# Optimization experiments

Measured on AMD Instinct MI355X. Metric: run time of the kernel, lower is better.

The kernel has to match this reference:

```python
import jax, jax.numpy as jnp
import numpy as np

B, T, C = 2, 2048, 2048
H, HKV = 32, 8
D = C // H            # head_dim = 64
G = H // HKV          # groups = 4
ROPE_BASE = 10000.0


def _rotate_half(x):
    x1, x2 = jnp.split(x, 2, axis=-1)
    return jnp.concatenate((-x2, x1), axis=-1)


def _rope_tables(seq_len, dim):
    inv_freq = 1.0 / (ROPE_BASE ** (jnp.arange(0, dim, 2, dtype=jnp.float32) / dim))
    t = jnp.arange(seq_len, dtype=jnp.float32)
    freqs = jnp.outer(t, inv_freq)          # [T, D/2]
    emb = jnp.concatenate((freqs, freqs), axis=-1)  # [T, D]
    return jnp.cos(emb), jnp.sin(emb)


def setup_inputs() -> dict:
    key = jax.random.key(0)
    ks = jax.random.split(key, 5)
    s = 0.02
    return {
        "x": jax.random.normal(ks[0], (B, T, C), jnp.float32),
        "Wq": jax.random.normal(ks[1], (C, C), jnp.float32) * s,
        "Wk": jax.random.normal(ks[2], (HKV * D, C), jnp.float32) * s,
        "Wv": jax.random.normal(ks[3], (HKV * D, C), jnp.float32) * s,
        "Wo": jax.random.normal(ks[4], (C, C), jnp.float32) * s,
    }


def reference(x, Wq, Wk, Wv, Wo):
    b, t, c = x.shape
    # fused QKV projections (nn.Linear: y = x @ W.T)
    q = (x @ Wq.T).reshape(b, t, H, D).transpose(0, 2, 1, 3)      # [B,H,T,D]
    k = (x @ Wk.T).reshape(b, t, HKV, D).transpose(0, 2, 1, 3)    # [B,HKV,T,D]
    v = (x @ Wv.T).reshape(b, t, HKV, D).transpose(0, 2, 1, 3)

    # RoPE (start_pos = 0)
    cos, sin = _rope_tables(t, D)           # [T, D] each
    cos = cos[None, None]                   # [1,1,T,D]
    sin = sin[None, None]
    q = q * cos + _rotate_half(q) * sin
    k = k * cos + _rotate_half(k) * sin

    # GQA head expansion (repeat_interleave on head dim)
    k = jnp.repeat(k, G, axis=1)            # [B,H,T,D]
    v = jnp.repeat(v, G, axis=1)

    # causal attention
    scale = 1.0 / jnp.sqrt(jnp.asarray(D, jnp.float32))
    scores = jnp.einsum('bhqd,bhkd->bhqk', q, k) * scale          # [B,H,T,T]
    causal = jnp.tril(jnp.ones((t, t), dtype=bool))
    scores = jnp.where(causal[None, None], scores, -jnp.inf)
    attn = jax.nn.softmax(scores.astype(jnp.float32), axis=-1).astype(q.dtype)
    out = jnp.einsum('bhqk,bhkd->bhqd', attn, v)                  # [B,H,T,D]
    out = out.transpose(0, 2, 1, 3).reshape(b, t, c)
    return out @ Wo.T
```

## Files before the change

### kernel.cpp

```cpp
#include <hip/hip_runtime.h>
#include <hip/hip_bf16.h>
#include <math.h>

typedef short short8 __attribute__((ext_vector_type(8)));
typedef float floatx4 __attribute__((ext_vector_type(4)));
typedef unsigned int uintx4 __attribute__((ext_vector_type(4)));
typedef int intx2 __attribute__((ext_vector_type(2)));

typedef __attribute__((address_space(1))) unsigned int as1_u32;
typedef __attribute__((address_space(3))) unsigned int as3_u32;

__device__ __forceinline__ void load_lds16(const void* g, void* l) {
  __builtin_amdgcn_global_load_lds((const as1_u32*)g, (as3_u32*)l, 16, 0, 0);
}

__device__ __forceinline__ unsigned short f2bf(float f) {
  __bf16 h = (__bf16)f;
  return __builtin_bit_cast(unsigned short, h);
}

__device__ __forceinline__ unsigned int pack_bf16(float a, float b) {
  return (unsigned int)f2bf(a) | ((unsigned int)f2bf(b) << 16);
}

#define TB 2
#define TT 2048
#define TC 2048
#define QKN 2560
#define KOFF 2048
#define SCALE_Q 0.18033688f

__global__ __launch_bounds__(256) void cast_all(
    const float* __restrict__ x, const float* __restrict__ wq,
    const float* __restrict__ wk, const float* __restrict__ wv,
    const float* __restrict__ wo,
    unsigned short* __restrict__ xb, unsigned short* __restrict__ wqkv,
    unsigned short* __restrict__ wob, float2* __restrict__ ropeTab) {
  if (blockIdx.x < 256) {
    const int idx = blockIdx.x * 256 + threadIdx.x;
    const int t = idx >> 5, d = idx & 31;
    const float inv = exp2f((float)d * -0.4152410119f);
    float sn, cs;
    sincosf((float)t * inv, &sn, &cs);
    ropeTab[idx] = make_float2(cs, sn);
  }
  long i4 = (long)blockIdx.x * 256 + threadIdx.x;
  const float* src;
  unsigned short* dst;
  if (i4 < 2097152)      { src = x;  dst = xb; }
  else if (i4 < 3145728) { src = wq; dst = wqkv;           i4 -= 2097152; }
  else if (i4 < 3407872) { src = wk; dst = wqkv + 4194304; i4 -= 3145728; }
  else if (i4 < 3670016) { src = wv; dst = wqkv + 5242880; i4 -= 3407872; }
  else                   { src = wo; dst = wob;            i4 -= 3670016; }
  float4 v = ((const float4*)src)[i4];
  ushort4 o;
  o.x = f2bf(v.x); o.y = f2bf(v.y); o.z = f2bf(v.z); o.w = f2bf(v.w);
  ((ushort4*)dst)[i4] = o;
}

__global__ __launch_bounds__(256) void gemm_qkv(const unsigned short* __restrict__ A,
                                                const unsigned short* __restrict__ Bw,
                                                unsigned short* __restrict__ qk,
                                                unsigned short* __restrict__ vT,
                                                const float2* __restrict__ ropeTab) {
  __shared__ unsigned short As[128 * 64];
  __shared__ unsigned short Bs[128 * 64];
  const int K = 2048;
  const int tid = threadIdx.x;
  const int lane = tid & 63, w = tid >> 6;
  const int quad = lane >> 4, l15 = lane & 15;
  const int wm = w >> 1, wn = w & 1;
  const int lin = blockIdx.y * 24 + blockIdx.x;
  const int sub = lin >> 3;
  const int m0 = (sub / 3) * 128;
  const int n0 = ((lin & 7) * 3 + sub % 3) * 128;

  floatx4 acc[4][4];
#pragma unroll
  for (int i = 0; i < 4; ++i)
#pragma unroll
    for (int j = 0; j < 4; ++j) acc[i][j] = (floatx4){0.f, 0.f, 0.f, 0.f};

  const int ar = tid >> 3;
  const int ac = (((tid & 7) ^ (ar & 7)) * 8);
  const unsigned short* Abase = A + (size_t)(m0 + ar) * K + ac;
  const unsigned short* Bbase = Bw + (size_t)(n0 + ar) * K + ac;

  for (int k0 = 0; k0 < K; k0 += 64) {
    __syncthreads();
#pragma unroll
    for (int p = 0; p < 4; ++p) {
      load_lds16(Abase + (size_t)(p * 32) * K + k0, (char*)As + p * 4096 + tid * 16);
      load_lds16(Bbase + (size_t)(p * 32) * K + k0, (char*)Bs + p * 4096 + tid * 16);
    }
    __syncthreads();
#pragma unroll
    for (int ks = 0; ks < 2; ++ks) {
      short8 af[4], bfr[4];
      const int key = (((ks << 2) + quad) ^ (l15 & 7)) << 4;
#pragma unroll
      for (int i = 0; i < 4; ++i)
        af[i] = *(const short8*)((const char*)As + (wm * 64 + i * 16 + l15) * 128 + key);
#pragma unroll
      for (int j = 0; j < 4; ++j)
        bfr[j] = *(const short8*)((const char*)Bs + (wn * 64 + j * 16 + l15) * 128 + key);
#pragma unroll
      for (int i = 0; i < 4; ++i)
#pragma unroll
        for (int j = 0; j < 4; ++j)
          acc[i][j] = __builtin_amdgcn_mfma_f32_16x16x32_bf16(af[i], bfr[j], acc[i][j], 0, 0, 0);
    }
  }

  const int colb = n0 + wn * 64;
  if (colb < QKN) {
    const float qscale = (colb < KOFF) ? SCALE_Q : 1.0f;
#pragma unroll
    for (int i = 0; i < 4; ++i) {
      const int rowb = m0 + wm * 64 + i * 16 + quad * 4;
      const int tb = rowb & (TT - 1);
#pragma unroll
      for (int j = 0; j < 2; ++j) {
        const int col = colb + j * 16 + l15;
        const int d = j * 16 + l15;
#pragma unroll
        for (int r = 0; r < 4; ++r) {
          const float2 cssn = ropeTab[(tb + r) * 32 + d];
          const float a = acc[i][j][r], b2 = acc[i][j + 2][r];
          const float qa = (a * cssn.x - b2 * cssn.y) * qscale;
          const float qb = (b2 * cssn.x + a * cssn.y) * qscale;
          unsigned short* p = qk + (size_t)(rowb + r) * QKN + col;
          p[0] = f2bf(qa);
          p[32] = f2bf(qb);
        }
      }
    }
  } else {
#pragma unroll
    for (int i = 0; i < 4; ++i) {
      const int rowb = m0 + wm * 64 + i * 16 + quad * 4;
#pragma unroll
      for (int j = 0; j < 4; ++j) {
        const int col = colb + j * 16 + l15;
        ushort4 pk;
        pk.x = f2bf(acc[i][j][0]); pk.y = f2bf(acc[i][j][1]);
        pk.z = f2bf(acc[i][j][2]); pk.w = f2bf(acc[i][j][3]);
        *(ushort4*)(vT + (size_t)(col - 2560) * 4096 + rowb) = pk;
      }
    }
  }
}

__global__ __launch_bounds__(256) void gemm_nt_f32(const unsigned short* __restrict__ A,
                                                   const unsigned short* __restrict__ Bw,
                                                   float* __restrict__ C,
                                                   int M, int N, int K) {
  __shared__ unsigned short As[128 * 64];
  __shared__ unsigned short Bs[128 * 64];
  const int tid = threadIdx.x;
  const int lane = tid & 63, w = tid >> 6;
  const int quad = lane >> 4, l15 = lane & 15;
  const int wm = w >> 1, wn = w & 1;
  const int lin = blockIdx.y * 16 + blockIdx.x;
  const int sub = lin >> 3;
  const int m0 = (sub >> 1) * 128;
  const int n0 = ((lin & 7) * 2 + (sub & 1)) * 128;

  floatx4 acc[4][4];
#pragma unroll
  for (int i = 0; i < 4; ++i)
#pragma unroll
    for (int j = 0; j < 4; ++j) acc[i][j] = (floatx4){0.f, 0.f, 0.f, 0.f};

  const int ar = tid >> 3;
  const int ac = (((tid & 7) ^ (ar & 7)) * 8);
  const unsigned short* Abase = A + (size_t)(m0 + ar) * K + ac;
  const unsigned short* Bbase = Bw + (size_t)(n0 + ar) * K + ac;

  for (int k0 = 0; k0 < K; k0 += 64) {
    __syncthreads();
#pragma unroll
    for (int p = 0; p < 4; ++p) {
      load_lds16(Abase + (size_t)(p * 32) * K + k0, (char*)As + p * 4096 + tid * 16);
      load_lds16(Bbase + (size_t)(p * 32) * K + k0, (char*)Bs + p * 4096 + tid * 16);
    }
    __syncthreads();
#pragma unroll
    for (int ks = 0; ks < 2; ++ks) {
      short8 af[4], bfr[4];
      const int key = (((ks << 2) + quad) ^ (l15 & 7)) << 4;
#pragma unroll
      for (int i = 0; i < 4; ++i)
        af[i] = *(const short8*)((const char*)As + (wm * 64 + i * 16 + l15) * 128 + key);
#pragma unroll
      for (int j = 0; j < 4; ++j)
        bfr[j] = *(const short8*)((const char*)Bs + (wn * 64 + j * 16 + l15) * 128 + key);
#pragma unroll
      for (int i = 0; i < 4; ++i)
#pragma unroll
        for (int j = 0; j < 4; ++j)
          acc[i][j] = __builtin_amdgcn_mfma_f32_16x16x32_bf16(af[i], bfr[j], acc[i][j], 0, 0, 0);
    }
  }
#pragma unroll
  for (int i = 0; i < 4; ++i) {
    const int row = m0 + wm * 64 + i * 16 + quad * 4;
#pragma unroll
    for (int j = 0; j < 4; ++j) {
      const int col = n0 + wn * 64 + j * 16 + l15;
#pragma unroll
      for (int r = 0; r < 4; ++r)
        C[(size_t)(row + r) * N + col] = acc[i][j][r];
    }
  }
}

__global__ __launch_bounds__(256, 3) void attn_kernel(const unsigned short* __restrict__ qk,
                                                      const unsigned short* __restrict__ vT,
                                                      unsigned short* __restrict__ attn) {
  const int h = blockIdx.x, b = blockIdx.y;
  const int qt = 15 - (int)blockIdx.z;
  const int hk = h >> 2;
  const int tid = threadIdx.x;
  const int w = tid >> 6, lane = tid & 63, quad = lane >> 4, l15 = lane & 15;

  __shared__ char lds[32768];

  const int srow = tid >> 3;
  const int sgrp = ((tid & 7) ^ (srow & 7));
  const int relbase = w * 32 + l15;

  const short8 ones = {16256, 16256, 16256, 16256, 16256, 16256, 16256, 16256};

  const size_t rowQ = (size_t)(b * TT + qt * 128);

  {
    const unsigned short* qsrc = qk + (rowQ + srow) * QKN + h * 64 + sgrp * 8;
#pragma unroll
    for (int p = 0; p < 4; ++p)
      load_lds16(qsrc + (size_t)p * 32 * QKN, lds + p * 4096 + tid * 16);
  }
  __syncthreads();
  short8 qf[2][2];
#pragma unroll
  for (int i = 0; i < 2; ++i)
#pragma unroll
    for (int ks = 0; ks < 2; ++ks)
      qf[i][ks] = *(const short8*)(lds + (w * 32 + i * 16 + l15) * 128 +
                                   ((((ks << 2) + quad) ^ (l15 & 7)) << 4));
  __syncthreads();

  floatx4 accO[2][4], accL[2];
#pragma unroll
  for (int i = 0; i < 2; ++i) {
    accL[i] = (floatx4){0.f, 0.f, 0.f, 0.f};
#pragma unroll
    for (int j = 0; j < 4; ++j) accO[i][j] = (floatx4){0.f, 0.f, 0.f, 0.f};
  }

  const unsigned short* kptr =
      qk + (size_t)(b * TT + srow) * QKN + KOFF + hk * 64 + sgrp * 8;
  const unsigned short* vptr =
      vT + (size_t)(hk * 64 + srow) * 4096 + b * TT + sgrp * 8;

  load_lds16(kptr, lds + tid * 16);
  load_lds16(kptr + (size_t)32 * QKN, lds + 4096 + tid * 16);
  load_lds16(vptr, lds + 16384 + tid * 16);
  load_lds16(vptr + (size_t)32 * 4096, lds + 16384 + 4096 + tid * 16);
  kptr += (size_t)64 * QKN;
  vptr += 64;
  __syncthreads();

  auto step = [&](const int BUF, const bool PREF, const int MREL) {
    if (PREF) {
      char* kd = lds + ((BUF ^ 1) * 8192);
      char* vd = lds + 16384 + ((BUF ^ 1) * 8192);
      load_lds16(kptr, kd + tid * 16);
      load_lds16(kptr + (size_t)32 * QKN, kd + 4096 + tid * 16);
      load_lds16(vptr, vd + tid * 16);
      load_lds16(vptr + (size_t)32 * 4096, vd + 4096 + tid * 16);
      kptr += (size_t)64 * QKN;
      vptr += 64;
    }

    const char* Ks = lds + BUF * 8192;
    floatx4 st[2][4];
    __builtin_amdgcn_s_setprio(1);
#pragma unroll
    for (int jm = 0; jm < 4; ++jm) {
      const int krow = jm * 16 + l15;
      const short8 kf0 = *(const short8*)(Ks + krow * 128 + ((quad ^ (l15 & 7)) << 4));
      const short8 kf1 = *(const short8*)(Ks + krow * 128 + (((4 + quad) ^ (l15 & 7)) << 4));
#pragma unroll
      for (int i = 0; i < 2; ++i) {
        floatx4 z = (floatx4){0.f, 0.f, 0.f, 0.f};
        z = __builtin_amdgcn_mfma_f32_16x16x32_bf16(kf0, qf[i][0], z, 0, 0, 0);
        st[i][jm] = __builtin_amdgcn_mfma_f32_16x16x32_bf16(kf1, qf[i][1], z, 0, 0, 0);
      }
    }
    __builtin_amdgcn_s_setprio(0);

    const char* Vt = lds + 16384 + BUF * 8192;
    short8 vf[2][4];
#pragma unroll
    for (int ks = 0; ks < 2; ++ks)
#pragma unroll
      for (int jd = 0; jd < 4; ++jd) {
        const int d = jd * 16 + l15;
        vf[ks][jd] = *(const short8*)(Vt + d * 128 +
                                      ((((ks << 2) + quad) ^ (l15 & 7)) << 4));
      }

    short8 pT[2][2];
#pragma unroll
    for (int i = 0; i < 2; ++i) {
      unsigned int U[4][2];
#pragma unroll
      for (int jm = 0; jm < 4; ++jm) {
        float e0 = exp2f(st[i][jm][0]);
        float e1 = exp2f(st[i][jm][1]);
        float e2 = exp2f(st[i][jm][2]);
        float e3 = exp2f(st[i][jm][3]);
        if (MREL >= 0) {
          const int rel = relbase + i * 16 - MREL;
          const int kg = jm * 16 + quad * 4;
          if (kg > rel) e0 = 0.f;
          if (kg + 1 > rel) e1 = 0.f;
          if (kg + 2 > rel) e2 = 0.f;
          if (kg + 3 > rel) e3 = 0.f;
        }
        U[jm][0] = pack_bf16(e0, e1);
        U[jm][1] = pack_bf16(e2, e3);
      }
#pragma unroll
      for (int ks = 0; ks < 2; ++ks) {
        uintx4 t;
#pragma unroll
        for (int hh = 0; hh < 2; ++hh) {
          intx2 r32 = __builtin_amdgcn_permlane32_swap(
              (int)U[2 * ks][hh], (int)U[2 * ks + 1][hh], false, false);
          intx2 r16 = __builtin_amdgcn_permlane16_swap(r32[0], r32[1], false, false);
          t[hh] = (unsigned int)r16[0];
          t[2 + hh] = (unsigned int)r16[1];
        }
        pT[i][ks] = __builtin_bit_cast(short8, t);
      }
    }

    __builtin_amdgcn_s_setprio(1);
#pragma unroll
    for (int ks = 0; ks < 2; ++ks) {
      accL[0] = __builtin_amdgcn_mfma_f32_16x16x32_bf16(pT[0][ks], ones, accL[0], 0, 0, 0);
      accL[1] = __builtin_amdgcn_mfma_f32_16x16x32_bf16(pT[1][ks], ones, accL[1], 0, 0, 0);
#pragma unroll
      for (int jd = 0; jd < 4; ++jd) {
        accO[0][jd] = __builtin_amdgcn_mfma_f32_16x16x32_bf16(pT[0][ks], vf[ks][jd], accO[0][jd], 0, 0, 0);
        accO[1][jd] = __builtin_amdgcn_mfma_f32_16x16x32_bf16(pT[1][ks], vf[ks][jd], accO[1][jd], 0, 0, 0);
      }
    }
    __builtin_amdgcn_s_setprio(0);
    __syncthreads();
  };

  for (int t2 = 0; t2 < qt; ++t2) {
    step(0, true, -1);
    step(1, true, -1);
  }
  step(0, true, 0);
  step(1, false, 64);

#pragma unroll
  for (int i2 = 0; i2 < 2; ++i2) {
#pragma unroll
    for (int jd = 0; jd < 4; ++jd) {
      const int col = h * 64 + jd * 16 + l15;
#pragma unroll
      for (int r = 0; r < 4; ++r) {
        const size_t row = rowQ + w * 32 + i2 * 16 + quad * 4 + r;
        attn[row * TC + col] = f2bf(accO[i2][jd][r] / accL[i2][r]);
      }
    }
  }
}

extern "C" void kernel_launch(void* const* d_in, const int* in_sizes, int n_in,
                              void* d_out, int out_size, void* d_ws, size_t ws_size,
                              hipStream_t stream) {
  const float* x = (const float*)d_in[0];
  const float* Wq = (const float*)d_in[1];
  const float* Wk = (const float*)d_in[2];
  const float* Wv = (const float*)d_in[3];
  const float* Wo = (const float*)d_in[4];
  float* out = (float*)d_out;

  char* ws = (char*)d_ws;
  unsigned short* xb   = (unsigned short*)(ws);
  unsigned short* wqkv = (unsigned short*)(ws + 16777216);
  unsigned short* wob  = (unsigned short*)(ws + 29360128);
  unsigned short* qk   = (unsigned short*)(ws + 37748736);
  unsigned short* vT   = (unsigned short*)(ws + 58720256);
  unsigned short* attn = (unsigned short*)(ws + 62914560);
  float2* ropeTab = (float2*)(ws + 62914560);

  cast_all<<<18432, 256, 0, stream>>>(x, Wq, Wk, Wv, Wo, xb, wqkv, wob, ropeTab);
  gemm_qkv<<<dim3(24, 32), 256, 0, stream>>>(xb, wqkv, qk, vT, ropeTab);
  attn_kernel<<<dim3(32, 2, 16), 256, 0, stream>>>(qk, vT, attn);
  gemm_nt_f32<<<dim3(16, 32), 256, 0, stream>>>(attn, wob, out, 4096, TC, 2048);
}
```

Baseline: 295.8 us.

## Rewrite projection GEMMs with 256x256 tiles and a 4-stage async LDS pipeline

Both the QKV and output-projection GEMMs move from 128x128 tiles with 256 threads and a single-buffered, two-barrier K loop to 256x256 tiles with 512 threads. They now use a four-buffer ring in 128KB of dynamic LDS, K-steps of 32, and `global_load_lds` prefetched three stages ahead. Explicit vmcnt waits and one barrier per stage replace the old sync pattern, and s_setprio raises wave priority around the MFMA blocks. The goal is to overlap global loads with MFMA work and cut LDS traffic per FLOP. The cost is far fewer workgroups (192 and 128) on a 256-CU part, so fewer CUs are kept busy.

```diff
diff --git a/kernel.cpp b/kernel.cpp
--- a/kernel.cpp
+++ b/kernel.cpp
@@ -58,66 +58,94 @@
   ((ushort4*)dst)[i4] = o;
 }
 
-__global__ __launch_bounds__(256) void gemm_qkv(const unsigned short* __restrict__ A,
-                                                const unsigned short* __restrict__ Bw,
-                                                unsigned short* __restrict__ qk,
-                                                unsigned short* __restrict__ vT,
-                                                const float2* __restrict__ ropeTab) {
-  __shared__ unsigned short As[128 * 64];
-  __shared__ unsigned short Bs[128 * 64];
-  const int K = 2048;
+
+__global__ __launch_bounds__(512, 2) void gemm_qkv(const unsigned short* __restrict__ A,
+                                                   const unsigned short* __restrict__ Bw,
+                                                   unsigned short* __restrict__ qk,
+                                                   unsigned short* __restrict__ vT,
+                                                   const float2* __restrict__ ropeTab) {
+  extern __shared__ char dynlds[];
+  const int K = 2048, NTILES = 64;
   const int tid = threadIdx.x;
   const int lane = tid & 63, w = tid >> 6;
   const int quad = lane >> 4, l15 = lane & 15;
-  const int wm = w >> 1, wn = w & 1;
-  const int lin = blockIdx.y * 24 + blockIdx.x;
-  const int sub = lin >> 3;
-  const int m0 = (sub / 3) * 128;
-  const int n0 = ((lin & 7) * 3 + sub % 3) * 128;
-
-  floatx4 acc[4][4];
-#pragma unroll
-  for (int i = 0; i < 4; ++i)
+  const int wm = w >> 2, wn = w & 3;
+
+  const int lin = blockIdx.y * 12 + blockIdx.x;
+  const int wg = (lin & 7) * 24 + (lin >> 3);
+  const int m0 = (wg / 12) * 256;
+  const int n0 = (wg % 12) * 256;
+
+  floatx4 acc[8][4];
+#pragma unroll
+  for (int i = 0; i < 8; ++i)
 #pragma unroll
     for (int j = 0; j < 4; ++j) acc[i][j] = (floatx4){0.f, 0.f, 0.f, 0.f};
 
-  const int ar = tid >> 3;
-  const int ac = (((tid & 7) ^ (ar & 7)) * 8);
-  const unsigned short* Abase = A + (size_t)(m0 + ar) * K + ac;
-  const unsigned short* Bbase = Bw + (size_t)(n0 + ar) * K + ac;
-
-  for (int k0 = 0; k0 < K; k0 += 64) {
-    __syncthreads();
-#pragma unroll
-    for (int p = 0; p < 4; ++p) {
-      load_lds16(Abase + (size_t)(p * 32) * K + k0, (char*)As + p * 4096 + tid * 16);
-      load_lds16(Bbase + (size_t)(p * 32) * K + k0, (char*)Bs + p * 4096 + tid * 16);
-    }
-    __syncthreads();
-#pragma unroll
-    for (int ks = 0; ks < 2; ++ks) {
-      short8 af[4], bfr[4];
-      const int key = (((ks << 2) + quad) ^ (l15 & 7)) << 4;
-#pragma unroll
-      for (int i = 0; i < 4; ++i)
-        af[i] = *(const short8*)((const char*)As + (wm * 64 + i * 16 + l15) * 128 + key);
+  const int srow = tid >> 2;
+  const int schk = (tid & 3) ^ (srow & 3);
+  const unsigned short* aS = A + (size_t)(m0 + srow) * K + schk * 8;
+  const unsigned short* bS = Bw + (size_t)(n0 + srow) * K + schk * 8;
+
+  const int rsw = (quad ^ (l15 & 3)) << 4;
+  const int rdA = (wm * 128 + l15) * 64 + rsw;
+  const int rdB = (wn * 64 + l15) * 64 + rsw;
+
+#pragma unroll
+  for (int tt = 0; tt < 3; ++tt) {
+    char* sb = dynlds + tt * 32768;
+    const unsigned short* aP = aS + (size_t)tt * 32;
+    const unsigned short* bP = bS + (size_t)tt * 32;
+    load_lds16(aP, sb + tid * 16);
+    load_lds16(aP + (size_t)128 * K, sb + 8192 + tid * 16);
+    load_lds16(bP, sb + 16384 + tid * 16);
+    load_lds16(bP + (size_t)128 * K, sb + 24576 + tid * 16);
+  }
+
+  auto kiter = [&](int t, const int VN, const bool ISSUE) {
+    if (VN == 8)      asm volatile("s_waitcnt vmcnt(8)" ::: "memory");
+    else if (VN == 4) asm volatile("s_waitcnt vmcnt(4)" ::: "memory");
+    else              asm volatile("s_waitcnt vmcnt(0)" ::: "memory");
+    __builtin_amdgcn_s_barrier();
+    asm volatile("" ::: "memory");
+    if (ISSUE) {
+      const int tt = t + 3;
+      char* sb = dynlds + (tt & 3) * 32768;
+      const unsigned short* aP = aS + (size_t)tt * 32;
+      const unsigned short* bP = bS + (size_t)tt * 32;
+      load_lds16(aP, sb + tid * 16);
+      load_lds16(aP + (size_t)128 * K, sb + 8192 + tid * 16);
+      load_lds16(bP, sb + 16384 + tid * 16);
+      load_lds16(bP + (size_t)128 * K, sb + 24576 + tid * 16);
+    }
+    const char* cb = dynlds + (t & 3) * 32768;
+    short8 af[8], bf[4];
+#pragma unroll
+    for (int i = 0; i < 8; ++i)
+      af[i] = *(const short8*)(cb + rdA + i * 1024);
+#pragma unroll
+    for (int j = 0; j < 4; ++j)
+      bf[j] = *(const short8*)(cb + 16384 + rdB + j * 1024);
+    __builtin_amdgcn_s_setprio(1);
+#pragma unroll
+    for (int i = 0; i < 8; ++i)
 #pragma unroll
       for (int j = 0; j < 4; ++j)
-        bfr[j] = *(const short8*)((const char*)Bs + (wn * 64 + j * 16 + l15) * 128 + key);
-#pragma unroll
-      for (int i = 0; i < 4; ++i)
-#pragma unroll
-        for (int j = 0; j < 4; ++j)
-          acc[i][j] = __builtin_amdgcn_mfma_f32_16x16x32_bf16(af[i], bfr[j], acc[i][j], 0, 0, 0);
-    }
-  }
+        acc[i][j] = __builtin_amdgcn_mfma_f32_16x16x32_bf16(af[i], bf[j], acc[i][j], 0, 0, 0);
+    __builtin_amdgcn_s_setprio(0);
+  };
+
+  for (int t = 0; t < NTILES - 3; ++t) kiter(t, 8, true);
+  kiter(NTILES - 3, 8, false);
+  kiter(NTILES - 2, 4, false);
+  kiter(NTILES - 1, 0, false);
 
   const int colb = n0 + wn * 64;
   if (colb < QKN) {
     const float qscale = (colb < KOFF) ? SCALE_Q : 1.0f;
 #pragma unroll
-    for (int i = 0; i < 4; ++i) {
-      const int rowb = m0 + wm * 64 + i * 16 + quad * 4;
+    for (int i = 0; i < 8; ++i) {
+      const int rowb = m0 + wm * 128 + i * 16 + quad * 4;
       const int tb = rowb & (TT - 1);
 #pragma unroll
       for (int j = 0; j < 2; ++j) {
@@ -137,8 +165,8 @@
     }
   } else {
 #pragma unroll
-    for (int i = 0; i < 4; ++i) {
-      const int rowb = m0 + wm * 64 + i * 16 + quad * 4;
+    for (int i = 0; i < 8; ++i) {
+      const int rowb = m0 + wm * 128 + i * 16 + quad * 4;
 #pragma unroll
       for (int j = 0; j < 4; ++j) {
         const int col = colb + j * 16 + l15;
@@ -151,60 +179,89 @@
   }
 }
 
-__global__ __launch_bounds__(256) void gemm_nt_f32(const unsigned short* __restrict__ A,
-                                                   const unsigned short* __restrict__ Bw,
-                                                   float* __restrict__ C,
-                                                   int M, int N, int K) {
-  __shared__ unsigned short As[128 * 64];
-  __shared__ unsigned short Bs[128 * 64];
+__global__ __launch_bounds__(512, 2) void gemm_nt_f32(const unsigned short* __restrict__ A,
+                                                      const unsigned short* __restrict__ Bw,
+                                                      float* __restrict__ C,
+                                                      int M, int N, int Kdim) {
+  extern __shared__ char dynlds[];
+  const int K = 2048, NTILES = 64;
   const int tid = threadIdx.x;
   const int lane = tid & 63, w = tid >> 6;
   const int quad = lane >> 4, l15 = lane & 15;
-  const int wm = w >> 1, wn = w & 1;
-  const int lin = blockIdx.y * 16 + blockIdx.x;
-  const int sub = lin >> 3;
-  const int m0 = (sub >> 1) * 128;
-  const int n0 = ((lin & 7) * 2 + (sub & 1)) * 128;
-
-  floatx4 acc[4][4];
-#pragma unroll
-  for (int i = 0; i < 4; ++i)
+  const int wm = w >> 2, wn = w & 3;
+
+  const int lin = blockIdx.y * 8 + blockIdx.x;
+  const int wg = (lin & 7) * 16 + (lin >> 3);
+  const int m0 = (wg >> 3) * 256;
+  const int n0 = (wg & 7) * 256;
+
+  floatx4 acc[8][4];
+#pragma unroll
+  for (int i = 0; i < 8; ++i)
 #pragma unroll
     for (int j = 0; j < 4; ++j) acc[i][j] = (floatx4){0.f, 0.f, 0.f, 0.f};
 
-  const int ar = tid >> 3;
-  const int ac = (((tid & 7) ^ (ar & 7)) * 8);
-  const unsigned short* Abase = A + (size_t)(m0 + ar) * K + ac;
-  const unsigned short* Bbase = Bw + (size_t)(n0 + ar) * K + ac;
-
-  for (int k0 = 0; k0 < K; k0 += 64) {
-    __syncthreads();
-#pragma unroll
-    for (int p = 0; p < 4; ++p) {
-      load_lds16(Abase + (size_t)(p * 32) * K + k0, (char*)As + p * 4096 + tid * 16);
-      load_lds16(Bbase + (size_t)(p * 32) * K + k0, (char*)Bs + p * 4096 + tid * 16);
-    }
-    __syncthreads();
-#pragma unroll
-    for (int ks = 0; ks < 2; ++ks) {
-      short8 af[4], bfr[4];
-      const int key = (((ks << 2) + quad) ^ (l15 & 7)) << 4;
-#pragma unroll
-      for (int i = 0; i < 4; ++i)
-        af[i] = *(const short8*)((const char*)As + (wm * 64 + i * 16 + l15) * 128 + key);
+  const int srow = tid >> 2;
+  const int schk = (tid & 3) ^ (srow & 3);
+  const unsigned short* aS = A + (size_t)(m0 + srow) * K + schk * 8;
+  const unsigned short* bS = Bw + (size_t)(n0 + srow) * K + schk * 8;
+
+  const int rsw = (quad ^ (l15 & 3)) << 4;
+  const int rdA = (wm * 128 + l15) * 64 + rsw;
+  const int rdB = (wn * 64 + l15) * 64 + rsw;
+
+#pragma unroll
+  for (int tt = 0; tt < 3; ++tt) {
+    char* sb = dynlds + tt * 32768;
+    const unsigned short* aP = aS + (size_t)tt * 32;
+    const unsigned short* bP = bS + (size_t)tt * 32;
+    load_lds16(aP, sb + tid * 16);
+    load_lds16(aP + (size_t)128 * K, sb + 8192 + tid * 16);
+    load_lds16(bP, sb + 16384 + tid * 16);
+    load_lds16(bP + (size_t)128 * K, sb + 24576 + tid * 16);
+  }
+
+  auto kiter = [&](int t, const int VN, const bool ISSUE) {
+    if (VN == 8)      asm volatile("s_waitcnt vmcnt(8)" ::: "memory");
+    else if (VN == 4) asm volatile("s_waitcnt vmcnt(4)" ::: "memory");
+    else              asm volatile("s_waitcnt vmcnt(0)" ::: "memory");
+    __builtin_amdgcn_s_barrier();
+    asm volatile("" ::: "memory");
+    if (ISSUE) {
+      const int tt = t + 3;
+      char* sb = dynlds + (tt & 3) * 32768;
+      const unsigned short* aP = aS + (size_t)tt * 32;
+      const unsigned short* bP = bS + (size_t)tt * 32;
+      load_lds16(aP, sb + tid * 16);
+      load_lds16(aP + (size_t)128 * K, sb + 8192 + tid * 16);
+      load_lds16(bP, sb + 16384 + tid * 16);
+      load_lds16(bP + (size_t)128 * K, sb + 24576 + tid * 16);
+    }
+    const char* cb = dynlds + (t & 3) * 32768;
+    short8 af[8], bf[4];
+#pragma unroll
+    for (int i = 0; i < 8; ++i)
+      af[i] = *(const short8*)(cb + rdA + i * 1024);
+#pragma unroll
+    for (int j = 0; j < 4; ++j)
+      bf[j] = *(const short8*)(cb + 16384 + rdB + j * 1024);
+    __builtin_amdgcn_s_setprio(1);
+#pragma unroll
+    for (int i = 0; i < 8; ++i)
 #pragma unroll
       for (int j = 0; j < 4; ++j)
-        bfr[j] = *(const short8*)((const char*)Bs + (wn * 64 + j * 16 + l15) * 128 + key);
-#pragma unroll
-      for (int i = 0; i < 4; ++i)
-#pragma unroll
-        for (int j = 0; j < 4; ++j)
-          acc[i][j] = __builtin_amdgcn_mfma_f32_16x16x32_bf16(af[i], bfr[j], acc[i][j], 0, 0, 0);
-    }
-  }
-#pragma unroll
-  for (int i = 0; i < 4; ++i) {
-    const int row = m0 + wm * 64 + i * 16 + quad * 4;
+        acc[i][j] = __builtin_amdgcn_mfma_f32_16x16x32_bf16(af[i], bf[j], acc[i][j], 0, 0, 0);
+    __builtin_amdgcn_s_setprio(0);
+  };
+
+  for (int t = 0; t < NTILES - 3; ++t) kiter(t, 8, true);
+  kiter(NTILES - 3, 8, false);
+  kiter(NTILES - 2, 4, false);
+  kiter(NTILES - 1, 0, false);
+
+#pragma unroll
+  for (int i = 0; i < 8; ++i) {
+    const int row = m0 + wm * 128 + i * 16 + quad * 4;
 #pragma unroll
     for (int j = 0; j < 4; ++j) {
       const int col = n0 + wn * 64 + j * 16 + l15;
@@ -403,7 +460,7 @@
   float2* ropeTab = (float2*)(ws + 62914560);
 
   cast_all<<<18432, 256, 0, stream>>>(x, Wq, Wk, Wv, Wo, xb, wqkv, wob, ropeTab);
-  gemm_qkv<<<dim3(24, 32), 256, 0, stream>>>(xb, wqkv, qk, vT, ropeTab);
+  gemm_qkv<<<dim3(12, 16), 512, 131072, stream>>>(xb, wqkv, qk, vT, ropeTab);
   attn_kernel<<<dim3(32, 2, 16), 256, 0, stream>>>(qk, vT, attn);
-  gemm_nt_f32<<<dim3(16, 32), 256, 0, stream>>>(attn, wob, out, 4096, TC, 2048);
-}
+  gemm_nt_f32<<<dim3(8, 16), 512, 131072, stream>>>(attn, wob, out, 4096, TC, 2048);
+}
```

New measurement: 299.2 us. About the same (+1.1%).

## Replace GEMMs with 256x256-tile double-buffered 8-wave phased MFMA pipeline

Applied to the files above, without the earlier changes.

Both projection GEMMs now share a helper that computes 256x256 output tiles with 512 threads. It double-buffers 128KB of dynamic LDS and splits each k-step into four phases, so global-to-LDS loads of the next tile overlap MFMA work on the current one, with explicit waitcnt, barriers and setprio. The larger tiles cut global traffic per flop, and the grid is remapped to match. The cost is far fewer workgroups (192 and 128 blocks), which may underfill the CUs, plus heavy register and LDS use and many barriers.

```diff
diff --git a/kernel.cpp b/kernel.cpp
--- a/kernel.cpp
+++ b/kernel.cpp
@@ -22,6 +22,8 @@
 __device__ __forceinline__ unsigned int pack_bf16(float a, float b) {
   return (unsigned int)f2bf(a) | ((unsigned int)f2bf(b) << 16);
 }
+
+#define MFMA16(a, b, c) __builtin_amdgcn_mfma_f32_16x16x32_bf16(a, b, c, 0, 0, 0)
 
 #define TB 2
 #define TT 2048
@@ -58,75 +60,167 @@
   ((ushort4*)dst)[i4] = o;
 }
 
-__global__ __launch_bounds__(256) void gemm_qkv(const unsigned short* __restrict__ A,
-                                                const unsigned short* __restrict__ Bw,
-                                                unsigned short* __restrict__ qk,
-                                                unsigned short* __restrict__ vT,
-                                                const float2* __restrict__ ropeTab) {
-  __shared__ unsigned short As[128 * 64];
-  __shared__ unsigned short Bs[128 * 64];
+__device__ __forceinline__ void gemm256_8ph(
+    const unsigned short* __restrict__ A, const unsigned short* __restrict__ Bw,
+    char* dynlds, int m0, int n0, int K, floatx4 (&acc)[8][4]) {
+  const int tid = threadIdx.x;
+  const int lane = tid & 63;
+  const int w = tid >> 6;
+  const int quad = lane >> 4, l15 = lane & 15;
+  const int wm = w >> 2, wn = w & 3;
+
+  const int srow8 = tid >> 3;
+  const int schk = (tid & 7) ^ (srow8 & 7);
+  const unsigned short* aS = A + (size_t)(m0 + srow8) * K + schk * 8;
+  const unsigned short* bS = Bw + (size_t)(n0 + srow8) * K + schk * 8;
+
+  const int key0 = (quad ^ (l15 & 7)) << 4;
+  const int key1 = ((4 + quad) ^ (l15 & 7)) << 4;
+  const int rdA = (wm * 16 + l15) * 128;
+  const int rdB = 32768 + ((wn >> 1) * 64 + (wn & 1) * 16 + l15) * 128;
+
+  const int NT = K >> 6;
+
+  auto stage = [&](int bb, int isB, int h, int tt) {
+    char* d = dynlds + bb * 65536 + isB * 32768 + h * 16384;
+    const unsigned short* s = (isB ? bS : aS) + (size_t)tt * 64 + (size_t)(h * 128) * K;
+    load_lds16(s, d + tid * 16);
+    load_lds16(s + (size_t)64 * K, d + 8192 + tid * 16);
+  };
+
+  stage(0, 0, 0, 0); stage(0, 1, 0, 0); stage(0, 1, 1, 0); stage(0, 0, 1, 0);
+  asm volatile("s_waitcnt vmcnt(4)" ::: "memory");
+  __builtin_amdgcn_s_barrier();
+
+  for (int t = 0; t < NT; ++t) {
+    const int b = t & 1, nb = b ^ 1;
+    const char* cb = dynlds + b * 65536;
+    const bool STG = (t < NT - 1);
+    short8 af[4][2], bfA[2][2], bfB[2][2];
+
+#pragma unroll
+    for (int i = 0; i < 4; ++i) {
+      af[i][0] = *(const short8*)(cb + rdA + i * 4096 + key0);
+      af[i][1] = *(const short8*)(cb + rdA + i * 4096 + key1);
+    }
+#pragma unroll
+    for (int j = 0; j < 2; ++j) {
+      bfA[j][0] = *(const short8*)(cb + rdB + j * 4096 + key0);
+      bfA[j][1] = *(const short8*)(cb + rdB + j * 4096 + key1);
+    }
+    if (STG) {
+      stage(nb, 0, 0, t + 1); stage(nb, 1, 0, t + 1);
+      asm volatile("s_waitcnt vmcnt(4)" ::: "memory");
+    } else {
+      asm volatile("s_waitcnt vmcnt(0)" ::: "memory");
+    }
+    __builtin_amdgcn_s_barrier();
+    asm volatile("s_waitcnt lgkmcnt(0)" ::: "memory");
+    __builtin_amdgcn_s_setprio(1);
+#pragma unroll
+    for (int i = 0; i < 4; ++i)
+#pragma unroll
+      for (int j = 0; j < 2; ++j) {
+        acc[i][j] = MFMA16(af[i][0], bfA[j][0], acc[i][j]);
+        acc[i][j] = MFMA16(af[i][1], bfA[j][1], acc[i][j]);
+      }
+    __builtin_amdgcn_s_setprio(0);
+    __builtin_amdgcn_s_barrier();
+
+#pragma unroll
+    for (int j = 0; j < 2; ++j) {
+      bfB[j][0] = *(const short8*)(cb + rdB + 16384 + j * 4096 + key0);
+      bfB[j][1] = *(const short8*)(cb + rdB + 16384 + j * 4096 + key1);
+    }
+    __builtin_amdgcn_s_barrier();
+    asm volatile("s_waitcnt lgkmcnt(0)" ::: "memory");
+    __builtin_amdgcn_s_setprio(1);
+#pragma unroll
+    for (int i = 0; i < 4; ++i)
+#pragma unroll
+      for (int j = 0; j < 2; ++j) {
+        acc[i][j + 2] = MFMA16(af[i][0], bfB[j][0], acc[i][j + 2]);
+        acc[i][j + 2] = MFMA16(af[i][1], bfB[j][1], acc[i][j + 2]);
+      }
+    __builtin_amdgcn_s_setprio(0);
+    __builtin_amdgcn_s_barrier();
+
+#pragma unroll
+    for (int i = 0; i < 4; ++i) {
+      af[i][0] = *(const short8*)(cb + rdA + (i + 4) * 4096 + key0);
+      af[i][1] = *(const short8*)(cb + rdA + (i + 4) * 4096 + key1);
+    }
+    if (STG) { stage(nb, 1, 1, t + 1); stage(nb, 0, 1, t + 1); }
+    __builtin_amdgcn_s_barrier();
+    asm volatile("s_waitcnt lgkmcnt(0)" ::: "memory");
+    __builtin_amdgcn_s_setprio(1);
+#pragma unroll
+    for (int i = 0; i < 4; ++i)
+#pragma unroll
+      for (int j = 0; j < 2; ++j) {
+        acc[i + 4][j + 2] = MFMA16(af[i][0], bfB[j][0], acc[i + 4][j + 2]);
+        acc[i + 4][j + 2] = MFMA16(af[i][1], bfB[j][1], acc[i + 4][j + 2]);
+      }
+    __builtin_amdgcn_s_setprio(0);
+    __builtin_amdgcn_s_barrier();
+
+    if (STG) asm volatile("s_waitcnt vmcnt(4)" ::: "memory");
+    __builtin_amdgcn_s_barrier();
+    __builtin_amdgcn_s_setprio(1);
+#pragma unroll
+    for (int i = 0; i < 4; ++i)
+#pragma unroll
+      for (int j = 0; j < 2; ++j) {
+        acc[i + 4][j] = MFMA16(af[i][0], bfA[j][0], acc[i + 4][j]);
+        acc[i + 4][j] = MFMA16(af[i][1], bfA[j][1], acc[i + 4][j]);
+      }
+    __builtin_amdgcn_s_setprio(0);
+    __builtin_amdgcn_s_barrier();
+  }
+}
+
+#define OUTCOL(n0, wn, j, l15) \
+  ((n0) + ((j) >> 1) * 128 + ((wn) >> 1) * 64 + ((wn) & 1) * 16 + ((j) & 1) * 32 + (l15))
+
+__global__ __launch_bounds__(512, 2) void gemm_qkv(const unsigned short* __restrict__ A,
+                                                   const unsigned short* __restrict__ Bw,
+                                                   unsigned short* __restrict__ qk,
+                                                   unsigned short* __restrict__ vT,
+                                                   const float2* __restrict__ ropeTab) {
+  extern __shared__ char dynlds[];
   const int K = 2048;
   const int tid = threadIdx.x;
   const int lane = tid & 63, w = tid >> 6;
   const int quad = lane >> 4, l15 = lane & 15;
-  const int wm = w >> 1, wn = w & 1;
-  const int lin = blockIdx.y * 24 + blockIdx.x;
-  const int sub = lin >> 3;
-  const int m0 = (sub / 3) * 128;
-  const int n0 = ((lin & 7) * 3 + sub % 3) * 128;
-
-  floatx4 acc[4][4];
-#pragma unroll
-  for (int i = 0; i < 4; ++i)
+  const int wm = w >> 2, wn = w & 3;
+
+  const int lin = blockIdx.y * 12 + blockIdx.x;
+  const int wg = (lin & 7) * 24 + (lin >> 3);
+  const int m0 = (wg / 12) * 256;
+  const int n0 = (wg % 12) * 256;
+
+  floatx4 acc[8][4];
+#pragma unroll
+  for (int i = 0; i < 8; ++i)
 #pragma unroll
     for (int j = 0; j < 4; ++j) acc[i][j] = (floatx4){0.f, 0.f, 0.f, 0.f};
 
-  const int ar = tid >> 3;
-  const int ac = (((tid & 7) ^ (ar & 7)) * 8);
-  const unsigned short* Abase = A + (size_t)(m0 + ar) * K + ac;
-  const unsigned short* Bbase = Bw + (size_t)(n0 + ar) * K + ac;
-
-  for (int k0 = 0; k0 < K; k0 += 64) {
-    __syncthreads();
-#pragma unroll
-    for (int p = 0; p < 4; ++p) {
-      load_lds16(Abase + (size_t)(p * 32) * K + k0, (char*)As + p * 4096 + tid * 16);
-      load_lds16(Bbase + (size_t)(p * 32) * K + k0, (char*)Bs + p * 4096 + tid * 16);
-    }
-    __syncthreads();
-#pragma unroll
-    for (int ks = 0; ks < 2; ++ks) {
-      short8 af[4], bfr[4];
-      const int key = (((ks << 2) + quad) ^ (l15 & 7)) << 4;
-#pragma unroll
-      for (int i = 0; i < 4; ++i)
-        af[i] = *(const short8*)((const char*)As + (wm * 64 + i * 16 + l15) * 128 + key);
-#pragma unroll
-      for (int j = 0; j < 4; ++j)
-        bfr[j] = *(const short8*)((const char*)Bs + (wn * 64 + j * 16 + l15) * 128 + key);
-#pragma unroll
-      for (int i = 0; i < 4; ++i)
-#pragma unroll
-        for (int j = 0; j < 4; ++j)
-          acc[i][j] = __builtin_amdgcn_mfma_f32_16x16x32_bf16(af[i], bfr[j], acc[i][j], 0, 0, 0);
-    }
-  }
-
-  const int colb = n0 + wn * 64;
-  if (colb < QKN) {
-    const float qscale = (colb < KOFF) ? SCALE_Q : 1.0f;
-#pragma unroll
-    for (int i = 0; i < 4; ++i) {
-      const int rowb = m0 + wm * 64 + i * 16 + quad * 4;
+  gemm256_8ph(A, Bw, dynlds, m0, n0, K, acc);
+
+  if (n0 < QKN) {
+    const float qscale = (n0 < KOFF) ? SCALE_Q : 1.0f;
+    const int d = (wn & 1) * 16 + l15;
+#pragma unroll
+    for (int i = 0; i < 8; ++i) {
+      const int rowb = m0 + i * 32 + wm * 16 + quad * 4;
       const int tb = rowb & (TT - 1);
 #pragma unroll
-      for (int j = 0; j < 2; ++j) {
-        const int col = colb + j * 16 + l15;
-        const int d = j * 16 + l15;
+      for (int jp = 0; jp < 4; jp += 2) {
+        const int col = OUTCOL(n0, wn, jp, l15);
 #pragma unroll
         for (int r = 0; r < 4; ++r) {
           const float2 cssn = ropeTab[(tb + r) * 32 + d];
-          const float a = acc[i][j][r], b2 = acc[i][j + 2][r];
+          const float a = acc[i][jp][r], b2 = acc[i][jp + 1][r];
           const float qa = (a * cssn.x - b2 * cssn.y) * qscale;
           const float qb = (b2 * cssn.x + a * cssn.y) * qscale;
           unsigned short* p = qk + (size_t)(rowb + r) * QKN + col;
@@ -137,11 +231,11 @@
     }
   } else {
 #pragma unroll
-    for (int i = 0; i < 4; ++i) {
-      const int rowb = m0 + wm * 64 + i * 16 + quad * 4;
+    for (int i = 0; i < 8; ++i) {
+      const int rowb = m0 + i * 32 + wm * 16 + quad * 4;
 #pragma unroll
       for (int j = 0; j < 4; ++j) {
-        const int col = colb + j * 16 + l15;
+        const int col = OUTCOL(n0, wn, j, l15);
         ushort4 pk;
         pk.x = f2bf(acc[i][j][0]); pk.y = f2bf(acc[i][j][1]);
         pk.z = f2bf(acc[i][j][2]); pk.w = f2bf(acc[i][j][3]);
@@ -151,63 +245,36 @@
   }
 }
 
-__global__ __launch_bounds__(256) void gemm_nt_f32(const unsigned short* __restrict__ A,
-                                                   const unsigned short* __restrict__ Bw,
-                                                   float* __restrict__ C,
-                                                   int M, int N, int K) {
-  __shared__ unsigned short As[128 * 64];
-  __shared__ unsigned short Bs[128 * 64];
+__global__ __launch_bounds__(512, 2) void gemm_nt_f32(const unsigned short* __restrict__ A,
+                                                      const unsigned short* __restrict__ Bw,
+                                                      float* __restrict__ C,
+                                                      int M, int N, int Kdim) {
+  extern __shared__ char dynlds[];
+  const int K = 2048;
   const int tid = threadIdx.x;
   const int lane = tid & 63, w = tid >> 6;
   const int quad = lane >> 4, l15 = lane & 15;
-  const int wm = w >> 1, wn = w & 1;
-  const int lin = blockIdx.y * 16 + blockIdx.x;
-  const int sub = lin >> 3;
-  const int m0 = (sub >> 1) * 128;
-  const int n0 = ((lin & 7) * 2 + (sub & 1)) * 128;
-
-  floatx4 acc[4][4];
-#pragma unroll
-  for (int i = 0; i < 4; ++i)
+  const int wm = w >> 2, wn = w & 3;
+
+  const int lin = blockIdx.y * 8 + blockIdx.x;
+  const int wg = (lin & 7) * 16 + (lin >> 3);
+  const int m0 = (wg >> 3) * 256;
+  const int n0 = (wg & 7) * 256;
+
+  floatx4 acc[8][4];
+#pragma unroll
+  for (int i = 0; i < 8; ++i)
 #pragma unroll
     for (int j = 0; j < 4; ++j) acc[i][j] = (floatx4){0.f, 0.f, 0.f, 0.f};
 
-  const int ar = tid >> 3;
-  const int ac = (((tid & 7) ^ (ar & 7)) * 8);
-  const unsigned short* Abase = A + (size_t)(m0 + ar) * K + ac;
-  const unsigned short* Bbase = Bw + (size_t)(n0 + ar) * K + ac;
-
-  for (int k0 = 0; k0 < K; k0 += 64) {
-    __syncthreads();
-#pragma unroll
-    for (int p = 0; p < 4; ++p) {
-      load_lds16(Abase + (size_t)(p * 32) * K + k0, (char*)As + p * 4096 + tid * 16);
-      load_lds16(Bbase + (size_t)(p * 32) * K + k0, (char*)Bs + p * 4096 + tid * 16);
-    }
-    __syncthreads();
-#pragma unroll
-    for (int ks = 0; ks < 2; ++ks) {
-      short8 af[4], bfr[4];
-      const int key = (((ks << 2) + quad) ^ (l15 & 7)) << 4;
-#pragma unroll
-      for (int i = 0; i < 4; ++i)
-        af[i] = *(const short8*)((const char*)As + (wm * 64 + i * 16 + l15) * 128 + key);
-#pragma unroll
-      for (int j = 0; j < 4; ++j)
-        bfr[j] = *(const short8*)((const char*)Bs + (wn * 64 + j * 16 + l15) * 128 + key);
-#pragma unroll
-      for (int i = 0; i < 4; ++i)
-#pragma unroll
-        for (int j = 0; j < 4; ++j)
-          acc[i][j] = __builtin_amdgcn_mfma_f32_16x16x32_bf16(af[i], bfr[j], acc[i][j], 0, 0, 0);
-    }
-  }
-#pragma unroll
-  for (int i = 0; i < 4; ++i) {
-    const int row = m0 + wm * 64 + i * 16 + quad * 4;
+  gemm256_8ph(A, Bw, dynlds, m0, n0, K, acc);
+
+#pragma unroll
+  for (int i = 0; i < 8; ++i) {
+    const int row = m0 + i * 32 + wm * 16 + quad * 4;
 #pragma unroll
     for (int j = 0; j < 4; ++j) {
-      const int col = n0 + wn * 64 + j * 16 + l15;
+      const int col = OUTCOL(n0, wn, j, l15);
 #pragma unroll
       for (int r = 0; r < 4; ++r)
         C[(size_t)(row + r) * N + col] = acc[i][j][r];
@@ -403,7 +470,7 @@
   float2* ropeTab = (float2*)(ws + 62914560);
 
   cast_all<<<18432, 256, 0, stream>>>(x, Wq, Wk, Wv, Wo, xb, wqkv, wob, ropeTab);
-  gemm_qkv<<<dim3(24, 32), 256, 0, stream>>>(xb, wqkv, qk, vT, ropeTab);
+  gemm_qkv<<<dim3(12, 16), 512, 131072, stream>>>(xb, wqkv, qk, vT, ropeTab);
   attn_kernel<<<dim3(32, 2, 16), 256, 0, stream>>>(qk, vT, attn);
-  gemm_nt_f32<<<dim3(16, 32), 256, 0, stream>>>(attn, wob, out, 4096, TC, 2048);
-}
+  gemm_nt_f32<<<dim3(8, 16), 512, 131072, stream>>>(attn, wob, out, 4096, TC, 2048);
+}
```

After: 287.8 us. 2.7% less time.
